# Kernel tuning notes

Measured on AMD Instinct MI355X. Metric: run time of the kernel, lower is better.

## Reference

```python
import jax, jax.numpy as jnp
import numpy as np

BOUNDS = 1.6  # aabb = [[b,b,b],[-b,-b,-b]]
C = 72       # output_coordinate_dim per plane


def _sample_planes(grids, coords):
    """Bilinear grid_sample, align_corners=True, padding_mode='border'.
    grids:  [P, C, H, W]
    coords: [P, N, 2] with (x, y) in [-1, 1]; x indexes W, y indexes H.
    returns [P, N, C]
    """
    P, Cc, H, W = grids.shape
    x = (coords[..., 0] + 1.0) * 0.5 * (W - 1)
    y = (coords[..., 1] + 1.0) * 0.5 * (H - 1)
    # border padding: clamp the sampling coordinate to the valid range
    x = jnp.clip(x, 0.0, W - 1)
    y = jnp.clip(y, 0.0, H - 1)
    x0 = jnp.floor(x)
    y0 = jnp.floor(y)
    wx = (x - x0)[..., None]  # [P, N, 1]
    wy = (y - y0)[..., None]
    x0i = x0.astype(jnp.int32)
    y0i = y0.astype(jnp.int32)
    x1i = jnp.minimum(x0i + 1, W - 1)
    y1i = jnp.minimum(y0i + 1, H - 1)

    def one_plane(g, y0i, y1i, x0i, x1i):
        # g: [C, H, W]; index tensors: [N] -> each gather [C, N] -> [N, C]
        v00 = g[:, y0i, x0i].T
        v01 = g[:, y0i, x1i].T
        v10 = g[:, y1i, x0i].T
        v11 = g[:, y1i, x1i].T
        return v00, v01, v10, v11

    v00, v01, v10, v11 = jax.vmap(one_plane)(grids, y0i, y1i, x0i, x1i)
    top = v00 * (1.0 - wx) + v01 * wx
    bot = v10 * (1.0 - wx) + v11 * wx
    return top * (1.0 - wy) + bot * wy  # [P, N, C]


def _triplane_forward(pts, grids_list):
    N = pts.shape[0]
    # normalize_aabb with aabb = [[b,b,b],[-b,-b,-b]]
    pts_n = (pts - BOUNDS) * (2.0 / (-BOUNDS - BOUNDS)) - 1.0  # == -pts / BOUNDS
    # plane coordinate combos: (0,1), (0,2), (1,2)
    coords = jnp.stack([pts_n[:, jnp.array([0, 1])],
                        pts_n[:, jnp.array([0, 2])],
                        pts_n[:, jnp.array([1, 2])]], axis=0)  # [3, N, 2]
    feats = []
    prev = None
    for g in grids_list:  # fixed small loop over scales
        samp = _sample_planes(g, coords)                 # [3, N, C]
        tri = samp.transpose(1, 0, 2).reshape(N, 3 * C)  # concat plane feats
        prev = tri if prev is None else tri + prev       # cumulative across scales
        feats.append(prev)
    return jnp.concatenate(feats, axis=-1)  # [N, 3*C*n_scales]


def setup_inputs() -> dict:
    key = jax.random.key(0)
    ks = jax.random.split(key, 5)
    N = 100000
    pts = jax.random.normal(ks[0], (N, 3), dtype=jnp.float32)
    resos = [64, 128, 256, 512]
    grids = {}
    for i, r in enumerate(resos):
        # original init is uniform(-0.01, 0.01)
        grids[f"grids_s{i}"] = jax.random.uniform(
            ks[i + 1], (3, C, r, r), dtype=jnp.float32, minval=-0.01, maxval=0.01)
    return {"pts": pts, **grids}


def reference(pts, grids_s0, grids_s1, grids_s2, grids_s3):
    return _triplane_forward(pts, [grids_s0, grids_s1, grids_s2, grids_s3])
```

## Files before the change

### kernel.cpp

```cpp
#include <hip/hip_runtime.h>


#define TP_C 72
#define TP_PLANES 3
#define TP_SCALES 4
#define TP_INV_BOUNDS 0.625f
#define TP_CVEC8 (TP_C / 8)

typedef float    tp_f4 __attribute__((ext_vector_type(4)));
typedef _Float16 tp_h4 __attribute__((ext_vector_type(4)));
typedef _Float16 tp_h8 __attribute__((ext_vector_type(8)));

#define TP_TILES0 96
#define TP_TILES1 480
#define TP_TILES2 2016
#define TP_TILES3 8160

#define TP_NBINS 32768

__global__ __launch_bounds__(256) void transpose_all_kernel(
    const float* __restrict__ g0, const float* __restrict__ g1,
    const float* __restrict__ g2, const float* __restrict__ g3,
    _Float16* __restrict__ t0, _Float16* __restrict__ t1,
    _Float16* __restrict__ t2, _Float16* __restrict__ t3)
{
    int b = blockIdx.x;
    const float* in;
    _Float16* out;
    int rr, tile;
    if (b < TP_TILES0)      { in = g0; out = t0; rr = 64 * 64;   tile = b; }
    else if (b < TP_TILES1) { in = g1; out = t1; rr = 128 * 128; tile = b - TP_TILES0; }
    else if (b < TP_TILES2) { in = g2; out = t2; rr = 256 * 256; tile = b - TP_TILES1; }
    else                    { in = g3; out = t3; rr = 512 * 512; tile = b - TP_TILES2; }

    int P0  = tile * 128;
    int p   = P0 / rr;
    int px0 = P0 - p * rr;

    __shared__ float lds[TP_C * 129];

    const float* inp = in + ((size_t)p * TP_C) * (size_t)rr + px0;
    int t = threadIdx.x;

    #pragma unroll
    for (int j = 0; j < 9; ++j) {
        int idx = j * 256 + t;
        int c   = idx >> 5;
        int q4  = idx & 31;
        tp_f4 v = __builtin_nontemporal_load(
            (const tp_f4*)(inp + (size_t)c * rr + q4 * 4));
        float* l = lds + c * 129 + q4 * 4;
        l[0] = v.x; l[1] = v.y; l[2] = v.z; l[3] = v.w;
    }
    __syncthreads();

    _Float16* outp = out + (size_t)P0 * TP_C;
    #pragma unroll
    for (int j = 0; j < 9; ++j) {
        int idx = j * 256 + t;
        int q   = idx / 18;
        int c4  = idx - q * 18;
        const float* l = lds + (c4 * 4) * 129 + q;
        tp_h4 hv;
        hv.x = (_Float16)l[0 * 129];
        hv.y = (_Float16)l[1 * 129];
        hv.z = (_Float16)l[2 * 129];
        hv.w = (_Float16)l[3 * 129];
        *(tp_h4*)(outp + (size_t)idx * 4) = hv;
    }
}

__device__ __forceinline__ unsigned tp_expand5(unsigned v) {
    unsigned r = (v & 1);
    r |= (v & 2)  << 2;
    r |= (v & 4)  << 4;
    r |= (v & 8)  << 6;
    r |= (v & 16) << 8;
    return r;
}

__global__ __launch_bounds__(256) void keys_kernel(
    const float* __restrict__ pts, unsigned* __restrict__ keys,
    unsigned* __restrict__ hist, int N)
{
    int n = blockIdx.x * 256 + threadIdx.x;
    if (n >= N) return;
    float nx = fminf(fmaxf(-pts[n * 3 + 0] * TP_INV_BOUNDS, -1.f), 1.f);
    float ny = fminf(fmaxf(-pts[n * 3 + 1] * TP_INV_BOUNDS, -1.f), 1.f);
    float nz = fminf(fmaxf(-pts[n * 3 + 2] * TP_INV_BOUNDS, -1.f), 1.f);
    int qx = min(31, max(0, (int)((nx + 1.f) * 16.f)));
    int qy = min(31, max(0, (int)((ny + 1.f) * 16.f)));
    int qz = min(31, max(0, (int)((nz + 1.f) * 16.f)));
    unsigned key = tp_expand5((unsigned)qx)
                 | (tp_expand5((unsigned)qy) << 1)
                 | (tp_expand5((unsigned)qz) << 2);
    keys[n] = key;
    atomicAdd(&hist[key], 1u);
}

__global__ __launch_bounds__(1024) void prefix_kernel(
    const unsigned* __restrict__ hist, unsigned* __restrict__ binoff)
{
    __shared__ unsigned part[1024];
    int t = threadIdx.x;
    unsigned local[32];
    unsigned s = 0;
    #pragma unroll
    for (int i = 0; i < 32; ++i) { local[i] = hist[t * 32 + i]; s += local[i]; }
    part[t] = s;
    __syncthreads();
    for (int off = 1; off < 1024; off <<= 1) {
        unsigned v = (t >= off) ? part[t - off] : 0u;
        __syncthreads();
        part[t] += v;
        __syncthreads();
    }
    unsigned run = (t == 0) ? 0u : part[t - 1];
    #pragma unroll
    for (int i = 0; i < 32; ++i) { binoff[t * 32 + i] = run; run += local[i]; }
}

__global__ __launch_bounds__(256) void scatter_kernel(
    const unsigned* __restrict__ keys, unsigned* __restrict__ binoff,
    unsigned* __restrict__ perm, int N)
{
    int n = blockIdx.x * 256 + threadIdx.x;
    if (n >= N) return;
    unsigned pos = atomicAdd(&binoff[keys[n]], 1u);
    perm[pos] = n;
}

__global__ __launch_bounds__(256) void triplane_gather_kernel(
    const float* __restrict__ pts,
    const unsigned* __restrict__ perm,
    const _Float16* __restrict__ t0,
    const _Float16* __restrict__ t1,
    const _Float16* __restrict__ t2,
    const _Float16* __restrict__ t3,
    float* __restrict__ out,
    int N)
{
    int idx = blockIdx.x * blockDim.x + threadIdx.x;
    int total = N * TP_PLANES * TP_CVEC8;
    if (idx >= total) return;

    int cv = idx % TP_CVEC8;
    int t  = idx / TP_CVEC8;
    int p  = t % TP_PLANES;
    int ns = t / TP_PLANES;
    int n  = (int)perm[ns];

    float nx = -pts[n * 3 + 0] * TP_INV_BOUNDS;
    float ny = -pts[n * 3 + 1] * TP_INV_BOUNDS;
    float nz = -pts[n * 3 + 2] * TP_INV_BOUNDS;

    float cx, cy;
    if (p == 0)      { cx = nx; cy = ny; }
    else if (p == 1) { cx = nx; cy = nz; }
    else             { cx = ny; cy = nz; }

    const _Float16* grids[TP_SCALES] = { t0, t1, t2, t3 };
    const int       res[TP_SCALES]   = { 64, 128, 256, 512 };

    float acc[8];
    #pragma unroll
    for (int k = 0; k < 8; ++k) acc[k] = 0.f;

    float* outrow = out + (size_t)n * (TP_SCALES * TP_PLANES * TP_C)
                        + (size_t)p * TP_C + cv * 8;

    #pragma unroll
    for (int s = 0; s < TP_SCALES; ++s) {
        const int r = res[s];
        const float rm1 = (float)(r - 1);

        float fx = (cx + 1.0f) * 0.5f * rm1;
        float fy = (cy + 1.0f) * 0.5f * rm1;
        fx = fminf(fmaxf(fx, 0.0f), rm1);
        fy = fminf(fmaxf(fy, 0.0f), rm1);

        float x0f = floorf(fx);
        float y0f = floorf(fy);
        float wx = fx - x0f;
        float wy = fy - y0f;
        int x0 = (int)x0f;
        int y0 = (int)y0f;
        int x1 = min(x0 + 1, r - 1);
        int y1 = min(y0 + 1, r - 1);

        const _Float16* g = grids[s] + ((size_t)p * r * r) * TP_C + (size_t)cv * 8;
        tp_h8 v00 = *(const tp_h8*)(g + ((size_t)y0 * r + x0) * TP_C);
        tp_h8 v01 = *(const tp_h8*)(g + ((size_t)y0 * r + x1) * TP_C);
        tp_h8 v10 = *(const tp_h8*)(g + ((size_t)y1 * r + x0) * TP_C);
        tp_h8 v11 = *(const tp_h8*)(g + ((size_t)y1 * r + x1) * TP_C);

        float iwx = 1.0f - wx;
        float iwy = 1.0f - wy;

        #pragma unroll
        for (int k = 0; k < 8; ++k) {
            float a00 = (float)v00[k];
            float a01 = (float)v01[k];
            float a10 = (float)v10[k];
            float a11 = (float)v11[k];
            float top = a00 * iwx + a01 * wx;
            float bot = a10 * iwx + a11 * wx;
            acc[k] += top * iwy + bot * wy;
        }

        tp_f4 lo = { acc[0], acc[1], acc[2], acc[3] };
        tp_f4 hi = { acc[4], acc[5], acc[6], acc[7] };
        float* orow = outrow + s * (TP_PLANES * TP_C);
        __builtin_nontemporal_store(lo, (tp_f4*)orow);
        __builtin_nontemporal_store(hi, (tp_f4*)(orow + 4));
    }
}

extern "C" void kernel_launch(void* const* d_in, const int* in_sizes, int n_in,
                              void* d_out, int out_size, void* d_ws, size_t ws_size,
                              hipStream_t stream) {
    const float* pts = (const float*)d_in[0];
    const float* g[TP_SCALES] = {
        (const float*)d_in[1], (const float*)d_in[2],
        (const float*)d_in[3], (const float*)d_in[4] };
    float* out = (float*)d_out;

    const int res[TP_SCALES] = { 64, 128, 256, 512 };
    int N = in_sizes[0] / 3;

    unsigned* hist   = (unsigned*)d_ws;
    unsigned* binoff = hist + TP_NBINS;
    unsigned* keys   = binoff + TP_NBINS;
    unsigned* perm   = keys + N;
    size_t meta = (size_t)2 * TP_NBINS + (size_t)2 * N;
    meta = (meta + 3) & ~(size_t)3;

    _Float16* tg[TP_SCALES];
    _Float16* tgbase = (_Float16*)((float*)d_ws + meta);
    size_t off = 0;
    for (int s = 0; s < TP_SCALES; ++s) {
        tg[s] = tgbase + off;
        off += (size_t)TP_PLANES * TP_C * res[s] * res[s];
    }

    (void)hipMemsetAsync(hist, 0, TP_NBINS * sizeof(unsigned), stream);

    int pblocks = (N + 255) / 256;
    keys_kernel<<<pblocks, 256, 0, stream>>>(pts, keys, hist, N);

    transpose_all_kernel<<<TP_TILES3, 256, 0, stream>>>(
        g[0], g[1], g[2], g[3], tg[0], tg[1], tg[2], tg[3]);

    prefix_kernel<<<1, 1024, 0, stream>>>(hist, binoff);
    scatter_kernel<<<pblocks, 256, 0, stream>>>(keys, binoff, perm, N);

    int total = N * TP_PLANES * TP_CVEC8;
    int block = 256;
    int grid = (total + block - 1) / block;
    triplane_gather_kernel<<<grid, block, 0, stream>>>(
        pts, perm, tg[0], tg[1], tg[2], tg[3], out, N);
}
```

Measured before the change: 691.0 us.

## Make gather plane-major with XCD-aware block remap and pre-sorted point records

Three changes. The scatter pass now writes sorted point records (xyz plus original index) so the gather no longer does an indirect perm lookup followed by a pts load. The gather's work order is now plane-major, so consecutive blocks touch only one plane's grid. Block IDs are also remapped so that each of the 8 XCDs processes a contiguous range of work, which is meant to improve L2 locality of grid texels. The trade-off is that output rows are written three times in separate passes per plane, which may reduce write coalescing.

```diff
diff --git a/kernel.cpp b/kernel.cpp
--- a/kernel.cpp
+++ b/kernel.cpp
@@ -6,6 +6,7 @@
 #define TP_SCALES 4
 #define TP_INV_BOUNDS 0.625f
 #define TP_CVEC8 (TP_C / 8)
+#define TP_NXCD 8
 
 typedef float    tp_f4 __attribute__((ext_vector_type(4)));
 typedef _Float16 tp_h4 __attribute__((ext_vector_type(4)));
@@ -121,38 +122,52 @@
 }
 
 __global__ __launch_bounds__(256) void scatter_kernel(
+    const float* __restrict__ pts,
     const unsigned* __restrict__ keys, unsigned* __restrict__ binoff,
-    unsigned* __restrict__ perm, int N)
+    float* __restrict__ spts, int N)
 {
     int n = blockIdx.x * 256 + threadIdx.x;
     if (n >= N) return;
     unsigned pos = atomicAdd(&binoff[keys[n]], 1u);
-    perm[pos] = n;
+    tp_f4 rec;
+    rec.x = pts[n * 3 + 0];
+    rec.y = pts[n * 3 + 1];
+    rec.z = pts[n * 3 + 2];
+    rec.w = __uint_as_float((unsigned)n);
+    *(tp_f4*)(spts + (size_t)pos * 4) = rec;
 }
 
 __global__ __launch_bounds__(256) void triplane_gather_kernel(
-    const float* __restrict__ pts,
-    const unsigned* __restrict__ perm,
+    const float* __restrict__ spts,
     const _Float16* __restrict__ t0,
     const _Float16* __restrict__ t1,
     const _Float16* __restrict__ t2,
     const _Float16* __restrict__ t3,
     float* __restrict__ out,
-    int N)
-{
-    int idx = blockIdx.x * blockDim.x + threadIdx.x;
-    int total = N * TP_PLANES * TP_CVEC8;
+    int N, int nwg)
+{
+    int orig = blockIdx.x;
+    int xcd  = orig % TP_NXCD;
+    int q    = nwg / TP_NXCD;
+    int r    = nwg % TP_NXCD;
+    int wgid = (xcd < r ? xcd * (q + 1) : r * (q + 1) + (xcd - r) * q) + orig / TP_NXCD;
+
+    int idx = wgid * 256 + (int)threadIdx.x;
+    int per_plane = N * TP_CVEC8;
+    int total = TP_PLANES * per_plane;
     if (idx >= total) return;
 
-    int cv = idx % TP_CVEC8;
-    int t  = idx / TP_CVEC8;
-    int p  = t % TP_PLANES;
-    int ns = t / TP_PLANES;
-    int n  = (int)perm[ns];
-
-    float nx = -pts[n * 3 + 0] * TP_INV_BOUNDS;
-    float ny = -pts[n * 3 + 1] * TP_INV_BOUNDS;
-    float nz = -pts[n * 3 + 2] * TP_INV_BOUNDS;
+    int p   = idx / per_plane;
+    int rem = idx - p * per_plane;
+    int ns  = rem / TP_CVEC8;
+    int cv  = rem - ns * TP_CVEC8;
+
+    tp_f4 sp = *(const tp_f4*)(spts + (size_t)ns * 4);
+    int n = (int)__float_as_uint(sp.w);
+
+    float nx = -sp.x * TP_INV_BOUNDS;
+    float ny = -sp.y * TP_INV_BOUNDS;
+    float nz = -sp.z * TP_INV_BOUNDS;
 
     float cx, cy;
     if (p == 0)      { cx = nx; cy = ny; }
@@ -171,8 +186,8 @@
 
     #pragma unroll
     for (int s = 0; s < TP_SCALES; ++s) {
-        const int r = res[s];
-        const float rm1 = (float)(r - 1);
+        const int r2 = res[s];
+        const float rm1 = (float)(r2 - 1);
 
         float fx = (cx + 1.0f) * 0.5f * rm1;
         float fy = (cy + 1.0f) * 0.5f * rm1;
@@ -185,14 +200,14 @@
         float wy = fy - y0f;
         int x0 = (int)x0f;
         int y0 = (int)y0f;
-        int x1 = min(x0 + 1, r - 1);
-        int y1 = min(y0 + 1, r - 1);
-
-        const _Float16* g = grids[s] + ((size_t)p * r * r) * TP_C + (size_t)cv * 8;
-        tp_h8 v00 = *(const tp_h8*)(g + ((size_t)y0 * r + x0) * TP_C);
-        tp_h8 v01 = *(const tp_h8*)(g + ((size_t)y0 * r + x1) * TP_C);
-        tp_h8 v10 = *(const tp_h8*)(g + ((size_t)y1 * r + x0) * TP_C);
-        tp_h8 v11 = *(const tp_h8*)(g + ((size_t)y1 * r + x1) * TP_C);
+        int x1 = min(x0 + 1, r2 - 1);
+        int y1 = min(y0 + 1, r2 - 1);
+
+        const _Float16* g = grids[s] + ((size_t)p * r2 * r2) * TP_C + (size_t)cv * 8;
+        tp_h8 v00 = *(const tp_h8*)(g + ((size_t)y0 * r2 + x0) * TP_C);
+        tp_h8 v01 = *(const tp_h8*)(g + ((size_t)y0 * r2 + x1) * TP_C);
+        tp_h8 v10 = *(const tp_h8*)(g + ((size_t)y1 * r2 + x0) * TP_C);
+        tp_h8 v11 = *(const tp_h8*)(g + ((size_t)y1 * r2 + x1) * TP_C);
 
         float iwx = 1.0f - wx;
         float iwy = 1.0f - wy;
@@ -231,8 +246,10 @@
     unsigned* hist   = (unsigned*)d_ws;
     unsigned* binoff = hist + TP_NBINS;
     unsigned* keys   = binoff + TP_NBINS;
-    unsigned* perm   = keys + N;
-    size_t meta = (size_t)2 * TP_NBINS + (size_t)2 * N;
+    size_t spts_off = (size_t)2 * TP_NBINS + (size_t)N;
+    spts_off = (spts_off + 3) & ~(size_t)3;
+    float* spts = (float*)d_ws + spts_off;
+    size_t meta = spts_off + (size_t)4 * N;
     meta = (meta + 3) & ~(size_t)3;
 
     _Float16* tg[TP_SCALES];
@@ -252,11 +269,11 @@
         g[0], g[1], g[2], g[3], tg[0], tg[1], tg[2], tg[3]);
 
     prefix_kernel<<<1, 1024, 0, stream>>>(hist, binoff);
-    scatter_kernel<<<pblocks, 256, 0, stream>>>(keys, binoff, perm, N);
-
-    int total = N * TP_PLANES * TP_CVEC8;
+    scatter_kernel<<<pblocks, 256, 0, stream>>>(pts, keys, binoff, spts, N);
+
+    int total = TP_PLANES * N * TP_CVEC8;
     int block = 256;
-    int grid = (total + block - 1) / block;
-    triplane_gather_kernel<<<grid, block, 0, stream>>>(
-        pts, perm, tg[0], tg[1], tg[2], tg[3], out, N);
-}
+    int nwg = (total + block - 1) / block;
+    triplane_gather_kernel<<<nwg, block, 0, stream>>>(
+        spts, tg[0], tg[1], tg[2], tg[3], out, N, nwg);
+}
```

Measured after the change: 757.5 us. 9.6% more time.
